# Optimization experiments

Measured on AMD Instinct MI355X. Metric: run time of the kernel, lower is better.

## Reference

```python
import jax, jax.numpy as jnp
import numpy as np

B, T, NE, NH, HD = 4, 1024, 768, 12, 64
CURV = 0.0
EPS = 1e-6
LN_EPS = 1e-5
ROPE_BASE = 10000.0


def project(x, k):
    # Lift Euclidean vector onto Lorentz hyperboloid with curvature K = exp(k):
    # time coord t = sqrt(K + ||x||^2) so that <lx, lx>_L = -K.
    K = jnp.exp(k)
    t = jnp.sqrt(K + jnp.sum(x * x, axis=-1, keepdims=True))
    return jnp.concatenate([t, x], axis=-1)


def lorentz_distance(lq, lk, k):
    # lq, lk: (B, H, T, D+1); k: (1, H, 1, 1) log-curvature.
    # d = sqrt(K) * arccosh(clamp(-<q,k>_L / K, 1+eps))
    K = jnp.exp(k)
    inner = (jnp.einsum('bhid,bhjd->bhij', lq[..., 1:], lk[..., 1:])
             - jnp.einsum('bhi,bhj->bhij', lq[..., 0], lk[..., 0]))
    c = jnp.clip(-inner / K, 1.0 + EPS, None)
    return jnp.sqrt(K) * jnp.arccosh(c)


def lorentz_norm(x):
    # sqrt(|<x,x>_L|) with <x,x>_L = -x0^2 + ||xs||^2  (keepdim)
    inner = -x[..., 0:1] ** 2 + jnp.sum(x[..., 1:] ** 2, axis=-1, keepdims=True)
    return jnp.sqrt(jnp.clip(-inner, EPS, None))


def rotary_tables():
    inv_freq = 1.0 / (ROPE_BASE ** (np.arange(0, HD, 2, dtype=np.float32) / HD))
    t = np.arange(T, dtype=np.float32)
    freqs = np.outer(t, inv_freq)  # (T, HD/2)
    cos = jnp.asarray(np.cos(freqs))[None, :, None, :]  # (1,T,1,HD/2)
    sin = jnp.asarray(np.sin(freqs))[None, :, None, :]
    return cos, sin


def apply_rotary(x, cos, sin):
    # x: (B, T, H, HD)
    x1, x2 = x[..., : HD // 2], x[..., HD // 2:]
    return jnp.concatenate([x1 * cos + x2 * sin, -x1 * sin + x2 * cos], axis=-1)


def layernorm(y, g, b):
    m = jnp.mean(y, axis=-1, keepdims=True)
    v = jnp.mean((y - m) ** 2, axis=-1, keepdims=True)
    return (y - m) / jnp.sqrt(v + LN_EPS) * g + b


def setup_inputs() -> dict:
    key = jax.random.key(0)
    ks = jax.random.split(key, 8)
    s = 0.02
    return {
        'x': jax.random.normal(ks[0], (B, T, NE), dtype=jnp.float32),
        'block_curvature': jnp.asarray(CURV, dtype=jnp.float32),
        'mlp_curvature': jnp.asarray(CURV, dtype=jnp.float32),
        'attn_curvatures': jnp.ones((1, NH, 1, 1), dtype=jnp.float32) * CURV,
        'qkv_w': jax.random.normal(ks[1], (3 * NE, NE + 1), dtype=jnp.float32) * s,
        'attn_proj_w': jax.random.normal(ks[2], (NE, (HD + 1) * NH), dtype=jnp.float32) * s,
        'attn_proj_b': jnp.zeros((NE,), dtype=jnp.float32),
        'mlp_expand_w': jax.random.normal(ks[3], (4 * NE + 3, NE + 1), dtype=jnp.float32) * s,
        'mlp_expand_b': jnp.zeros((4 * NE + 3,), dtype=jnp.float32),
        'mlp_shrink_w': jax.random.normal(ks[4], (NE, 4 * (NE + 1)), dtype=jnp.float32) * s,
        'mlp_shrink_b': jnp.zeros((NE,), dtype=jnp.float32),
        'ln_g': jnp.ones((NE,), dtype=jnp.float32),
        'ln_b': jnp.zeros((NE,), dtype=jnp.float32),
    }


def reference(x, block_curvature, mlp_curvature, attn_curvatures, qkv_w,
              attn_proj_w, attn_proj_b, mlp_expand_w, mlp_expand_b,
              mlp_shrink_w, mlp_shrink_b, ln_g, ln_b):
    cos, sin = rotary_tables()
    causal_bias = jnp.where(
        jnp.triu(jnp.ones((T, T), dtype=bool), k=1), -jnp.inf, 0.0).astype(jnp.float32)

    def block_norm(lx):
        return project(layernorm(lx[..., 1:], ln_g, ln_b), block_curvature)

    def attn(lx):
        qkv = lx @ qkv_w.T  # (B, T, 3*NE)
        q, k, v = jnp.split(qkv, 3, axis=-1)
        q = apply_rotary(q.reshape(B, T, NH, HD), cos, sin)
        k = apply_rotary(k.reshape(B, T, NH, HD), cos, sin)
        v = v.reshape(B, T, NH, HD)
        lq = project(q.transpose(0, 2, 1, 3), attn_curvatures)  # (B,H,T,HD+1)
        lk = project(k.transpose(0, 2, 1, 3), attn_curvatures)
        lv = project(v.transpose(0, 2, 1, 3), attn_curvatures)
        dis = lorentz_distance(lq, lk, attn_curvatures)  # (B,H,T,T)
        aw = jax.nn.softmax(-dis + causal_bias, axis=-1)
        a = jnp.einsum('bhij,bhjd->bhid', aw, lv)  # (B,H,T,HD+1)
        a = a * jnp.sqrt(jnp.exp(attn_curvatures)) / lorentz_norm(a)
        a = a.transpose(0, 2, 1, 3).reshape(B, T, NH * (HD + 1))
        a = a @ attn_proj_w.T + attn_proj_b
        return project(a, block_curvature)

    def mlp(lx):
        h = lx @ mlp_expand_w.T + mlp_expand_b  # (B,T,4*NE+3)
        h = project(h, mlp_curvature)[..., 1:]  # drop time coord back to 4*NE+3
        h = jax.nn.gelu(h, approximate=False)
        h = project(h, mlp_curvature)  # (B,T,4*(NE+1))
        h = h @ mlp_shrink_w.T + mlp_shrink_b
        return project(h, block_curvature)

    def skip(lx, f_lx):
        return project(lx[..., 1:] + f_lx[..., 1:], block_curvature)

    lx = project(x, block_curvature)  # (B,T,NE+1)
    lx = skip(lx, attn(block_norm(lx)))
    lx = skip(lx, mlp(block_norm(lx)))
    return lx
```

## Files before the change

kernel.cpp:

```cpp
#include <hip/hip_runtime.h>
#include <cmath>

typedef unsigned short ushort_t;
typedef __attribute__((ext_vector_type(8))) short short8;
typedef __attribute__((ext_vector_type(4))) float floatx4;

#define NH    12
#define T     1024
#define ROWS  4096
#define NE    768
#define KPA   832
#define KPB   3136
#define NEXP  3200
#define HEXP  3075
#define NSPLIT 3

__device__ __forceinline__ ushort_t f2bf(float f) {
  union { float f; unsigned u; } v; v.f = f;
  unsigned r = v.u + 0x7fffu + ((v.u >> 16) & 1u);
  return (ushort_t)(r >> 16);
}
__device__ __forceinline__ ushort_t f2bf_trunc(float f) {
  union { float f; unsigned u; } v; v.f = f;
  return (ushort_t)(v.u >> 16);
}
__device__ __forceinline__ float bf2f(ushort_t b) {
  union { unsigned u; float f; } v; v.u = ((unsigned)b) << 16;
  return v.f;
}
__device__ __forceinline__ float blk_reduce_sum(float v, float* sm) {
  #pragma unroll
  for (int o = 32; o > 0; o >>= 1) v += __shfl_xor(v, o, 64);
  int lane = threadIdx.x & 63, w = threadIdx.x >> 6;
  __syncthreads();
  if (lane == 0) sm[w] = v;
  __syncthreads();
  return sm[0] + sm[1] + sm[2] + sm[3];
}
__device__ __forceinline__ float red16_sum(float v) {
  #pragma unroll
  for (int o = 1; o < 16; o <<= 1) v += __shfl_xor(v, o, 64);
  return v;
}

#define NB_A 7488
#define NB_B 2496
#define NB_C 10400
#define NB_D 9408
#define NB_E 16
__device__ __forceinline__ void cvt_elem(ushort_t* __restrict__ dst,
                                         const float* __restrict__ src,
                                         int idx, int srcRows, int srcK, int dstK) {
  int r = idx / dstK, c = idx - r * dstK;
  dst[idx] = (r < srcRows && c < srcK) ? f2bf(src[(size_t)r * srcK + c]) : (ushort_t)0;
}
__global__ __launch_bounds__(256) void prep_kernel(
    ushort_t* __restrict__ qkv_wb, const float* __restrict__ qkvw,
    ushort_t* __restrict__ proj_wb, const float* __restrict__ projw,
    ushort_t* __restrict__ exp_wb, const float* __restrict__ expw,
    ushort_t* __restrict__ shr_wb, const float* __restrict__ shrw,
    ushort_t* __restrict__ aout_bf,
    const float* __restrict__ xin, const float* __restrict__ g,
    const float* __restrict__ bb, const float* __restrict__ curv,
    ushort_t* __restrict__ lnp) {
  __shared__ float sm[4];
  int blk = blockIdx.x;
  int tid = threadIdx.x;
  if (blk < NB_A) {
    cvt_elem(qkv_wb, qkvw, blk * 256 + tid, 2304, 769, KPA);
  } else if (blk < NB_A + NB_B) {
    cvt_elem(proj_wb, projw, (blk - NB_A) * 256 + tid, 768, 780, KPA);
  } else if (blk < NB_A + NB_B + NB_C) {
    cvt_elem(exp_wb, expw, (blk - NB_A - NB_B) * 256 + tid, HEXP, 769, KPA);
  } else if (blk < NB_A + NB_B + NB_C + NB_D) {
    cvt_elem(shr_wb, shrw, (blk - NB_A - NB_B - NB_C) * 256 + tid, 768, 3076, KPB);
  } else if (blk < NB_A + NB_B + NB_C + NB_D + NB_E) {
    int r = (blk - NB_A - NB_B - NB_C - NB_D) * 256 + tid;
    ushort_t* p = aout_bf + (size_t)r * KPA + 780;
    #pragma unroll
    for (int j = 0; j < KPA - 780; ++j) p[j] = 0;
  } else {
    const int row = blk - (NB_A + NB_B + NB_C + NB_D + NB_E);
    const float* xr = xin + (size_t)row * NE;
    float xv[3];
    float s = 0.f, ss = 0.f;
    #pragma unroll
    for (int i = 0; i < 3; ++i) {
      xv[i] = xr[tid + 256 * i];
      s += xv[i]; ss += xv[i] * xv[i];
    }
    s = blk_reduce_sum(s, sm);
    ss = blk_reduce_sum(ss, sm);
    float mean = s * (1.f / 768.f);
    float var = ss * (1.f / 768.f) - mean * mean;
    float rstd = rsqrtf(var + 1e-5f);
    float yv[3]; float ys = 0.f;
    #pragma unroll
    for (int i = 0; i < 3; ++i) {
      int c = tid + 256 * i;
      yv[i] = (xv[i] - mean) * rstd * g[c] + bb[c];
      ys += yv[i] * yv[i];
    }
    ys = blk_reduce_sum(ys, sm);
    float tc = sqrtf(expf(curv[0]) + ys);
    ushort_t* orow = lnp + (size_t)row * KPA;
    #pragma unroll
    for (int i = 0; i < 3; ++i) orow[1 + tid + 256 * i] = f2bf(yv[i]);
    if (tid == 0) orow[0] = f2bf(tc);
    if (tid < KPA - 769) orow[769 + tid] = 0;
  }
}

__global__ __launch_bounds__(256) void gemm_bf16(
    const ushort_t* __restrict__ A, int lda,
    const ushort_t* __restrict__ W, int ldw,
    void* __restrict__ Cout, int ldc,
    int nkTot, int cpt,
    const float* __restrict__ bias, int biasN,
    const float* __restrict__ res, int ldres,
    int outMode, void* __restrict__ Cp) {
  __shared__ ushort_t As[128 * 64];
  __shared__ ushort_t Bs[128 * 64];
  const int tid = threadIdx.x;
  const int w = tid >> 6, lane = tid & 63;

  int bx = blockIdx.x, by = blockIdx.y;
  {
    const int gx = gridDim.x, gy = gridDim.y;
    const int nwg = gx * gy;
    if ((nwg & 7) == 0) {
      int lin = by * gx + bx;
      int swz = (lin & 7) * (nwg >> 3) + (lin >> 3);
      bx = swz % gx;
      by = swz / gx;
    }
  }
  const int rowBase = by << 7;
  const int colBase = bx << 7;
  const int wm = (w & 1) * 64, wn = (w >> 1) * 64;
  const int lm = lane & 15, quad = lane >> 4;
  const int p0 = quad ^ (lm & 7);

  floatx4 acc[4][4];
  #pragma unroll
  for (int i = 0; i < 4; ++i)
    #pragma unroll
    for (int j = 0; j < 4; ++j) {
      floatx4 z = {0.f, 0.f, 0.f, 0.f};
      acc[i][j] = z;
    }

  const int kt0 = (int)blockIdx.z * cpt;
  const int kt1 = min(nkTot, kt0 + cpt);
  for (int kt = kt0; kt < kt1; ++kt) {
    __syncthreads();
    #pragma unroll
    for (int j = 0; j < 4; ++j) {
      int ci = j * 256 + tid;
      int r = ci >> 3;
      int g = (ci & 7) ^ (r & 7);
      const ushort_t* ga = A + (size_t)(rowBase + r) * lda + kt * 64 + g * 8;
      const ushort_t* gb = W + (size_t)(colBase + r) * ldw + kt * 64 + g * 8;
      __builtin_amdgcn_global_load_lds(
          (const __attribute__((address_space(1))) void*)ga,
          (__attribute__((address_space(3))) void*)&As[(j * 256 + w * 64) * 8],
          16, 0, 0);
      __builtin_amdgcn_global_load_lds(
          (const __attribute__((address_space(1))) void*)gb,
          (__attribute__((address_space(3))) void*)&Bs[(j * 256 + w * 64) * 8],
          16, 0, 0);
    }
    __syncthreads();

    #pragma unroll
    for (int s = 0; s < 2; ++s) {
      const int ps = s ? (p0 ^ 4) : p0;
      short8 af[4], bfr[4];
      #pragma unroll
      for (int i = 0; i < 4; ++i) {
        af[i]  = *(const short8*)&As[(wm + i * 16 + lm) * 64 + ps * 8];
        bfr[i] = *(const short8*)&Bs[(wn + i * 16 + lm) * 64 + ps * 8];
      }
      #pragma unroll
      for (int i = 0; i < 4; ++i)
        #pragma unroll
        for (int jn = 0; jn < 4; ++jn)
          acc[i][jn] = __builtin_amdgcn_mfma_f32_16x16x32_bf16(
              af[i], bfr[jn], acc[i][jn], 0, 0, 0);
    }
  }

  if (gridDim.z > 1) {
    ushort_t* dst = (ushort_t*)Cp + (size_t)blockIdx.z * ROWS * ldc;
    #pragma unroll
    for (int i = 0; i < 4; ++i)
      #pragma unroll
      for (int jn = 0; jn < 4; ++jn) {
        const int col = colBase + wn + jn * 16 + lm;
        #pragma unroll
        for (int rg = 0; rg < 4; ++rg) {
          const int row = rowBase + wm + i * 16 + quad * 4 + rg;
          dst[(size_t)row * ldc + col] = f2bf(acc[i][jn][rg]);
        }
      }
  } else if (outMode == 1) {
    ushort_t* C = (ushort_t*)Cout;
    #pragma unroll
    for (int i = 0; i < 4; ++i)
      #pragma unroll
      for (int jn = 0; jn < 4; ++jn) {
        const int col = colBase + wn + jn * 16 + lm;
        const float bv = bias ? ((col < biasN) ? bias[col] : 0.f) : 0.f;
        #pragma unroll
        for (int rg = 0; rg < 4; ++rg) {
          const int row = rowBase + wm + i * 16 + quad * 4 + rg;
          C[(size_t)row * ldc + col] = f2bf(acc[i][jn][rg] + bv);
        }
      }
  } else {
    float* C = (float*)Cout;
    #pragma unroll
    for (int i = 0; i < 4; ++i)
      #pragma unroll
      for (int jn = 0; jn < 4; ++jn) {
        const int col = colBase + wn + jn * 16 + lm;
        const float bv = bias ? ((col < biasN) ? bias[col] : 0.f) : 0.f;
        #pragma unroll
        for (int rg = 0; rg < 4; ++rg) {
          const int row = rowBase + wm + i * 16 + quad * 4 + rg;
          float o = acc[i][jn][rg] + bv;
          if (res) o += res[(size_t)row * ldres + col];
          C[(size_t)row * ldc + col] = o;
        }
      }
  }
}

__global__ __launch_bounds__(256) void rope_project(
    const ushort_t* __restrict__ qkv, const float* __restrict__ ac,
    ushort_t* __restrict__ qb, ushort_t* __restrict__ kb, ushort_t* __restrict__ vtb,
    float* __restrict__ q0, float* __restrict__ k0, float* __restrict__ v0) {
  int gid = blockIdx.x * 4 + (threadIdx.x >> 6);
  int lane = threadIdx.x & 63;
  int h = gid % NH;
  int bt = gid / NH;
  int t = bt & (T - 1);
  int b = bt >> 10;
  size_t base = (size_t)bt * 2304 + h * 64;
  float qv = bf2f(qkv[base + lane]);
  float kv = bf2f(qkv[base + 768 + lane]);
  float vv = bf2f(qkv[base + 1536 + lane]);
  int f = lane & 31;
  float ang = (float)t * __builtin_amdgcn_exp2f(-(float)f * 0.4152410118661534f);
  float sn, cs;
  sincosf(ang, &sn, &cs);
  float qp = __shfl(qv, lane ^ 32, 64);
  float kp = __shfl(kv, lane ^ 32, 64);
  float qr = (lane < 32) ? (qv * cs + qp * sn) : (-qp * sn + qv * cs);
  float kr = (lane < 32) ? (kv * cs + kp * sn) : (-kp * sn + kv * cs);
  float Kh = expf(ac[h]);
  float sq = qr * qr, sk = kr * kr, sv = vv * vv;
  #pragma unroll
  for (int o = 32; o > 0; o >>= 1) {
    sq += __shfl_xor(sq, o, 64);
    sk += __shfl_xor(sk, o, 64);
    sv += __shfl_xor(sv, o, 64);
  }
  size_t idx = ((size_t)(b * NH + h) * T + t);
  qb[idx * 64 + lane] = f2bf(qr);
  kb[idx * 64 + lane] = f2bf(kr);
  vtb[(size_t)(b * NH + h) * (64 * T) + (size_t)lane * T + t] = f2bf(vv);
  if (lane == 0) {
    q0[idx] = sqrtf(Kh + sq);
    k0[idx] = sqrtf(Kh + sk);
    v0[idx] = sqrtf(Kh + sv);
  }
}

__global__ __launch_bounds__(512, 4) void attn_kernel(
    const ushort_t* __restrict__ qb, const ushort_t* __restrict__ kb,
    const ushort_t* __restrict__ vtb,
    const float* __restrict__ q0, const float* __restrict__ k0,
    const float* __restrict__ v0,
    const float* __restrict__ ac,
    ushort_t* __restrict__ Opart, float* __restrict__ lpart,
    float* __restrict__ a0part) {
  __shared__ ushort_t QP[8 * 1152];
  __shared__ ushort_t Ks[2][64 * 64];
  __shared__ ushort_t Vts[2][64 * 64];

  const int sIdx = blockIdx.x;
  const int qtile = (int)gridDim.y - 1 - (int)blockIdx.y;
  const int bh = blockIdx.z;
  const int h = bh % NH;
  const int qt0 = qtile * 128;
  const int tid = threadIdx.x;
  const int w = tid >> 6, lane = tid & 63;
  const int lm = lane & 15, quad = lane >> 4;
  const int wm = w * 16;
  const int sw = lm & 7;
  const int preg = w * 1152;

  const int n = 2 * qtile + 2;
  const int kbeg = (n * sIdx) / NSPLIT;
  const int kend = (n * (sIdx + 1)) / NSPLIT;
  const size_t pb = (size_t)(sIdx * 48 + bh) * T;

  if (kbeg >= kend) {
    #pragma unroll
    for (int r = 0; r < 4; ++r) {
      const int i = qt0 + wm + quad * 4 + r;
      ushort_t* orow = Opart + (pb + i) * 64;
      #pragma unroll
      for (int nt = 0; nt < 4; ++nt) orow[nt * 16 + lm] = 0;
      if (lm == 0) { lpart[pb + i] = 0.f; a0part[pb + i] = 0.f; }
    }
    return;
  }

  const float Kh = expf(ac[h]);
  const float sqrtK = sqrtf(Kh);
  const float invK = 1.0f / Kh;
  const float nsK = -sqrtK;
  const bool k1 = (Kh == 1.0f);

  {
    const ushort_t* qtp = qb + ((size_t)bh * T + qt0) * 64;
    #pragma unroll
    for (int j = 0; j < 2; ++j) {
      int g = j * 8 + w;
      int ci = g * 64 + lane;
      int r = ci >> 3;
      int clog = ((ci & 7) ^ (r & 7)) * 8;
      __builtin_amdgcn_global_load_lds(
          (const __attribute__((address_space(1))) void*)(qtp + r * 64 + clog),
          (__attribute__((address_space(3))) void*)&QP[(g >> 1) * 1152 + (g & 1) * 512],
          16, 0, 0);
    }
  }
  const ushort_t* kbase = kb + (size_t)bh * T * 64;
  const ushort_t* vbh = vtb + (size_t)bh * (64 * T);
  const float* k0row = k0 + (size_t)bh * T;
  const float* v0row = v0 + (size_t)bh * T;
  const int ldr = tid >> 3;
  const int ldcs = ((tid & 7) ^ (ldr & 7)) * 8;
  {
    const int j0 = kbeg * 64;
    __builtin_amdgcn_global_load_lds(
        (const __attribute__((address_space(1))) void*)(kbase + (size_t)(j0 + ldr) * 64 + ldcs),
        (__attribute__((address_space(3))) void*)&Ks[0][w * 512], 16, 0, 0);
    __builtin_amdgcn_global_load_lds(
        (const __attribute__((address_space(1))) void*)(vbh + (size_t)ldr * T + j0 + ldcs),
        (__attribute__((address_space(3))) void*)&Vts[0][w * 512], 16, 0, 0);
  }
  float k0n[4], v0n[4];
  #pragma unroll
  for (int jt = 0; jt < 4; ++jt) {
    k0n[jt] = k0row[kbeg * 64 + jt * 16 + lm];
    v0n[jt] = v0row[kbeg * 64 + jt * 16 + lm];
  }
  float q0rv[4];
  #pragma unroll
  for (int r = 0; r < 4; ++r)
    q0rv[r] = q0[(size_t)bh * T + qt0 + wm + quad * 4 + r];

  asm volatile("s_waitcnt vmcnt(0)" ::: "memory");
  __builtin_amdgcn_s_barrier();
  __builtin_amdgcn_sched_barrier(0);

  short8 qf0 = *(const short8*)&QP[preg + lm * 64 + ((0 + quad) ^ sw) * 8];
  short8 qf1 = *(const short8*)&QP[preg + lm * 64 + ((4 + quad) ^ sw) * 8];
  asm volatile("" : "+v"(qf0), "+v"(qf1));

  float lsum[4], a0r[4];
  floatx4 oacc[4];
  #pragma unroll
  for (int r = 0; r < 4; ++r) { lsum[r] = 0.f; a0r[r] = 0.f; }
  #pragma unroll
  for (int nt = 0; nt < 4; ++nt) { floatx4 z = {0.f,0.f,0.f,0.f}; oacc[nt] = z; }

  int cur = 0;
  for (int kt = kbeg; kt < kend; ++kt) {
    const bool hasNext = (kt + 1 < kend);
    float k0i[4], v0v[4];
    #pragma unroll
    for (int jt = 0; jt < 4; ++jt) { k0i[jt] = k0n[jt] * invK; v0v[jt] = v0n[jt]; }

    if (hasNext) {
      const int j0n = (kt + 1) * 64;
      __builtin_amdgcn_global_load_lds(
          (const __attribute__((address_space(1))) void*)(kbase + (size_t)(j0n + ldr) * 64 + ldcs),
          (__attribute__((address_space(3))) void*)&Ks[cur ^ 1][w * 512], 16, 0, 0);
      __builtin_amdgcn_global_load_lds(
          (const __attribute__((address_space(1))) void*)(vbh + (size_t)ldr * T + j0n + ldcs),
          (__attribute__((address_space(3))) void*)&Vts[cur ^ 1][w * 512], 16, 0, 0);
      #pragma unroll
      for (int jt = 0; jt < 4; ++jt) {
        k0n[jt] = k0row[j0n + jt * 16 + lm];
        v0n[jt] = v0row[j0n + jt * 16 + lm];
      }
    }

    const int j0 = kt * 64;
    const ushort_t* Kc = Ks[cur];
    const ushort_t* Vc = Vts[cur];

    floatx4 sacc[4];
    __builtin_amdgcn_s_setprio(1);
    #pragma unroll
    for (int jt = 0; jt < 4; ++jt) {
      const int krow = jt * 16 + lm;
      short8 kf0 = *(const short8*)&Kc[krow * 64 + ((0 + quad) ^ sw) * 8];
      short8 kf1 = *(const short8*)&Kc[krow * 64 + ((4 + quad) ^ sw) * 8];
      floatx4 z = {0.f, 0.f, 0.f, 0.f};
      z = __builtin_amdgcn_mfma_f32_16x16x32_bf16(qf0, kf0, z, 0, 0, 0);
      z = __builtin_amdgcn_mfma_f32_16x16x32_bf16(qf1, kf1, z, 0, 0, 0);
      sacc[jt] = z;
    }
    __builtin_amdgcn_s_setprio(0);

    const bool maskT = (kt >= 2 * qtile);
    if (k1) {
      #pragma unroll
      for (int r = 0; r < 4; ++r) {
        const int i = qt0 + wm + quad * 4 + r;
        float ls = 0.f, a0s = 0.f;
        #pragma unroll
        for (int jt = 0; jt < 4; ++jt) {
          float c = fmaf(-invK, sacc[jt][r], q0rv[r] * k0i[jt]);
          c = fmaxf(c, 1.000001f);
          float p = c - sqrtf(fmaf(c, c, -1.f));
          if (maskT && (j0 + jt * 16 + lm > i)) p = 0.f;
          ushort_t pb2 = f2bf_trunc(p);
          QP[preg + (quad * 4 + r) * 72 + jt * 16 + lm] = pb2;
          float pf = bf2f(pb2);
          ls += pf;
          a0s = fmaf(pf, v0v[jt], a0s);
        }
        lsum[r] += ls;
        a0r[r] += a0s;
      }
    } else {
      #pragma unroll
      for (int r = 0; r < 4; ++r) {
        const int i = qt0 + wm + quad * 4 + r;
        float ls = 0.f, a0s = 0.f;
        #pragma unroll
        for (int jt = 0; jt < 4; ++jt) {
          float c = fmaf(-invK, sacc[jt][r], q0rv[r] * k0i[jt]);
          c = fmaxf(c, 1.000001f);
          float z = c + sqrtf(fmaf(c, c, -1.f));
          float p = __builtin_amdgcn_exp2f(nsK * __builtin_amdgcn_logf(z));
          if (maskT && (j0 + jt * 16 + lm > i)) p = 0.f;
          ushort_t pb2 = f2bf_trunc(p);
          QP[preg + (quad * 4 + r) * 72 + jt * 16 + lm] = pb2;
          float pf = bf2f(pb2);
          ls += pf;
          a0s = fmaf(pf, v0v[jt], a0s);
        }
        lsum[r] += ls;
        a0r[r] += a0s;
      }
    }

    short8 pf0 = *(const short8*)&QP[preg + lm * 72 + quad * 8];
    short8 pf1 = *(const short8*)&QP[preg + lm * 72 + 32 + quad * 8];
    __builtin_amdgcn_s_setprio(1);
    #pragma unroll
    for (int nt = 0; nt < 4; ++nt) {
      const int vrow = nt * 16 + lm;
      short8 vf0 = *(const short8*)&Vc[vrow * 64 + ((0 + quad) ^ sw) * 8];
      short8 vf1 = *(const short8*)&Vc[vrow * 64 + ((4 + quad) ^ sw) * 8];
      oacc[nt] = __builtin_amdgcn_mfma_f32_16x16x32_bf16(pf0, vf0, oacc[nt], 0, 0, 0);
      oacc[nt] = __builtin_amdgcn_mfma_f32_16x16x32_bf16(pf1, vf1, oacc[nt], 0, 0, 0);
    }
    __builtin_amdgcn_s_setprio(0);

    if (hasNext) {
      asm volatile("s_waitcnt vmcnt(0)" ::: "memory");
      __builtin_amdgcn_s_barrier();
      __builtin_amdgcn_sched_barrier(0);
    }
    cur ^= 1;
  }

  #pragma unroll
  for (int r = 0; r < 4; ++r) {
    float lf = red16_sum(lsum[r]);
    float a0f = red16_sum(a0r[r]);
    const int i = qt0 + wm + quad * 4 + r;
    ushort_t* orow = Opart + (pb + i) * 64;
    #pragma unroll
    for (int nt = 0; nt < 4; ++nt) orow[nt * 16 + lm] = f2bf(oacc[nt][r]);
    if (lm == 0) { lpart[pb + i] = lf; a0part[pb + i] = a0f; }
  }
}

__global__ __launch_bounds__(256) void attn_combine(
    const ushort_t* __restrict__ Opart, const float* __restrict__ lpart,
    const float* __restrict__ a0part,
    const float* __restrict__ ac, ushort_t* __restrict__ aout) {
  const int widx = blockIdx.x * 4 + (threadIdx.x >> 6);
  const int lane = threadIdx.x & 63;
  const int bh = widx >> 10;
  const int t = widx & 1023;
  const int h = bh % NH, b = bh / NH;
  float L = 0.f, A0 = 0.f, O = 0.f;
  #pragma unroll
  for (int sp = 0; sp < NSPLIT; ++sp) {
    const size_t r = (size_t)(sp * 48 + bh) * T + t;
    L += lpart[r];
    A0 += a0part[r];
    O += bf2f(Opart[r * 64 + lane]);
  }
  const float invl = 1.f / L;
  float av = O * invl;
  float ssq = av * av;
  #pragma unroll
  for (int o = 32; o > 0; o >>= 1) ssq += __shfl_xor(ssq, o, 64);
  float a0n = A0 * invl;
  float nsq = fmaxf(a0n * a0n - ssq, 1e-6f);
  float Kh = expf(ac[h]);
  float scale = sqrtf(Kh) * rsqrtf(nsq);
  ushort_t* orow = aout + (size_t)(b * T + t) * KPA + h * 65;
  orow[1 + lane] = f2bf(av * scale);
  if (lane == 0) orow[0] = f2bf(a0n * scale);
}

__global__ __launch_bounds__(256) void gelu_project(
    const ushort_t* __restrict__ hsrc, const float* __restrict__ curv,
    ushort_t* __restrict__ hp) {
  __shared__ float sm[4];
  const int row = blockIdx.x;
  const int tid = threadIdx.x;
  const ushort_t* hr = hsrc + (size_t)row * NEXP;
  float gv[13];
  float ss = 0.f;
  #pragma unroll
  for (int i = 0; i < 13; ++i) {
    int c = tid + 256 * i;
    float xx = (c < HEXP) ? bf2f(hr[c]) : 0.f;
    float gg = 0.5f * xx * (1.f + erff(xx * 0.70710678118654752f));
    gv[i] = gg; ss += gg * gg;
  }
  ss = blk_reduce_sum(ss, sm);
  float tc = sqrtf(expf(curv[0]) + ss);
  ushort_t* orow = hp + (size_t)row * KPB;
  #pragma unroll
  for (int i = 0; i < 13; ++i) {
    int c = tid + 256 * i;
    if (c < HEXP) orow[1 + c] = f2bf(gv[i]);
  }
  if (tid == 0) orow[0] = f2bf(tc);
  if (tid < KPB - (HEXP + 1)) orow[HEXP + 1 + tid] = 0;
}

__global__ __launch_bounds__(256) void reduce_ln_project(
    const ushort_t* __restrict__ Cp, int nsplit,
    const float* __restrict__ bias, const float* __restrict__ res,
    float* __restrict__ x2out,
    const float* __restrict__ g, const float* __restrict__ bb,
    const float* __restrict__ curv, ushort_t* __restrict__ lnp) {
  __shared__ float sm[4];
  const int row = blockIdx.x;
  const int tid = threadIdx.x;
  float xv[3];
  float s = 0.f, ss = 0.f;
  #pragma unroll
  for (int i = 0; i < 3; ++i) {
    const int c = tid + 256 * i;
    float v = bias[c] + res[(size_t)row * NE + c];
    for (int sp = 0; sp < nsplit; ++sp)
      v += bf2f(Cp[(size_t)sp * ROWS * NE + (size_t)row * NE + c]);
    x2out[(size_t)row * NE + c] = v;
    xv[i] = v;
    s += v; ss += v * v;
  }
  s = blk_reduce_sum(s, sm);
  ss = blk_reduce_sum(ss, sm);
  float mean = s * (1.f / 768.f);
  float var = ss * (1.f / 768.f) - mean * mean;
  float rstd = rsqrtf(var + 1e-5f);
  float yv[3]; float ys = 0.f;
  #pragma unroll
  for (int i = 0; i < 3; ++i) {
    int c = tid + 256 * i;
    yv[i] = (xv[i] - mean) * rstd * g[c] + bb[c];
    ys += yv[i] * yv[i];
  }
  ys = blk_reduce_sum(ys, sm);
  float tc = sqrtf(expf(curv[0]) + ys);
  ushort_t* orow = lnp + (size_t)row * KPA;
  #pragma unroll
  for (int i = 0; i < 3; ++i) orow[1 + tid + 256 * i] = f2bf(yv[i]);
  if (tid == 0) orow[0] = f2bf(tc);
  if (tid < KPA - 769) orow[769 + tid] = 0;
}

__global__ __launch_bounds__(256) void reduce_final_project(
    const ushort_t* __restrict__ Cp, int nsplit,
    const float* __restrict__ bias, const float* __restrict__ res,
    const float* __restrict__ curv, float* __restrict__ out) {
  __shared__ float sm[4];
  const int row = blockIdx.x;
  const int tid = threadIdx.x;
  float v[3]; float ss = 0.f;
  #pragma unroll
  for (int i = 0; i < 3; ++i) {
    const int c = tid + 256 * i;
    float t = bias[c] + res[(size_t)row * NE + c];
    for (int sp = 0; sp < nsplit; ++sp)
      t += bf2f(Cp[(size_t)sp * ROWS * NE + (size_t)row * NE + c]);
    v[i] = t; ss += t * t;
  }
  ss = blk_reduce_sum(ss, sm);
  float tc = sqrtf(expf(curv[0]) + ss);
  float* o = out + (size_t)row * 769;
  #pragma unroll
  for (int i = 0; i < 3; ++i) o[1 + tid + 256 * i] = v[i];
  if (tid == 0) o[0] = tc;
}

extern "C" void kernel_launch(void* const* d_in, const int* in_sizes, int n_in,
                              void* d_out, int out_size, void* d_ws, size_t ws_size,
                              hipStream_t stream) {
  (void)in_sizes; (void)n_in; (void)out_size; (void)ws_size;
  const float* x     = (const float*)d_in[0];
  const float* bc    = (const float*)d_in[1];
  const float* mc    = (const float*)d_in[2];
  const float* ac    = (const float*)d_in[3];
  const float* qkvw  = (const float*)d_in[4];
  const float* projw = (const float*)d_in[5];
  const float* projb = (const float*)d_in[6];
  const float* expw  = (const float*)d_in[7];
  const float* expb  = (const float*)d_in[8];
  const float* shrw  = (const float*)d_in[9];
  const float* shrb  = (const float*)d_in[10];
  const float* lng   = (const float*)d_in[11];
  const float* lnb   = (const float*)d_in[12];
  float* out = (float*)d_out;

  float* x2 = (float*)d_ws;
  ushort_t* qkv_wb  = (ushort_t*)(x2 + (size_t)ROWS * NE);
  ushort_t* proj_wb = qkv_wb + (size_t)2304 * KPA;
  ushort_t* exp_wb  = proj_wb + (size_t)768 * KPA;
  ushort_t* shr_wb  = exp_wb + (size_t)NEXP * KPA;
  ushort_t* lnp_bf  = shr_wb + (size_t)768 * KPB;
  ushort_t* aout_bf = lnp_bf + (size_t)ROWS * KPA;
  char* r2 = (char*)(aout_bf + (size_t)ROWS * KPA);
  ushort_t* qkvb = (ushort_t*)r2;
  ushort_t* qbb = qkvb + (size_t)ROWS * 2304;
  ushort_t* kbb = qbb + (size_t)48 * T * 64;
  ushort_t* vtb = kbb + (size_t)48 * T * 64;
  float* q0b = (float*)(vtb + (size_t)48 * T * 64);
  float* k0b = q0b + (size_t)48 * T;
  float* v0b = k0b + (size_t)48 * T;
  ushort_t* Opart = (ushort_t*)(v0b + (size_t)48 * T);
  float* lpart = (float*)(Opart + (size_t)NSPLIT * 48 * T * 64);
  float* a0part = lpart + (size_t)NSPLIT * 48 * T;
  ushort_t* ppartP = (ushort_t*)r2;
  ushort_t* hbbf = (ushort_t*)r2;
  ushort_t* hp_bf = hbbf + (size_t)ROWS * NEXP;
  ushort_t* ppartS = hp_bf + (size_t)ROWS * KPB;

  prep_kernel<<<NB_A + NB_B + NB_C + NB_D + NB_E + ROWS, 256, 0, stream>>>(
      qkv_wb, qkvw, proj_wb, projw, exp_wb, expw, shr_wb, shrw, aout_bf,
      x, lng, lnb, bc, lnp_bf);
  gemm_bf16<<<dim3(2304 / 128, ROWS / 128, 1), 256, 0, stream>>>(
      lnp_bf, KPA, qkv_wb, KPA, qkvb, 2304, KPA / 64, KPA / 64,
      nullptr, 0, nullptr, 0, 1, nullptr);
  rope_project<<<(ROWS * NH) / 4, 256, 0, stream>>>(qkvb, ac, qbb, kbb, vtb, q0b, k0b, v0b);
  attn_kernel<<<dim3(NSPLIT, T / 128, 48), 512, 0, stream>>>(
      qbb, kbb, vtb, q0b, k0b, v0b, ac, Opart, lpart, a0part);
  attn_combine<<<(48 * T) / 4, 256, 0, stream>>>(Opart, lpart, a0part, ac, aout_bf);
  gemm_bf16<<<dim3(768 / 128, ROWS / 128, 2), 256, 0, stream>>>(
      aout_bf, KPA, proj_wb, KPA, nullptr, NE, KPA / 64, 7,
      nullptr, 0, nullptr, 0, 0, ppartP);
  reduce_ln_project<<<ROWS, 256, 0, stream>>>(
      ppartP, 2, projb, x, x2, lng, lnb, bc, lnp_bf);
  gemm_bf16<<<dim3(NEXP / 128, ROWS / 128, 1), 256, 0, stream>>>(
      lnp_bf, KPA, exp_wb, KPA, hbbf, NEXP, KPA / 64, KPA / 64,
      expb, HEXP, nullptr, 0, 1, nullptr);
  gelu_project<<<ROWS, 256, 0, stream>>>(hbbf, mc, hp_bf);
  gemm_bf16<<<dim3(768 / 128, ROWS / 128, 4), 256, 0, stream>>>(
      hp_bf, KPB, shr_wb, KPB, nullptr, NE, KPB / 64, 13,
      nullptr, 0, nullptr, 0, 0, ppartS);
  reduce_final_project<<<ROWS, 256, 0, stream>>>(
      ppartS, 4, shrb, x2, bc, out);
}
```

Before: 369.3 us.

## Load K/V fragments directly from global memory, drop LDS double buffering and barriers

The attention kernel no longer stages K and V^T tiles through double-buffered shared memory. Each wave now reads its MFMA K and V fragments straight from global memory (relying on L1/L2 reuse across waves) and loads only its own Q rows, which removes all block-wide barriers. This shrinks LDS use and synchronisation, but adds latency-exposed global loads with no prefetch, and the 8 waves re-read the same K/V data. The occupancy hint in launch_bounds is also removed.

```diff
diff --git a/kernel.cpp b/kernel.cpp
--- a/kernel.cpp
+++ b/kernel.cpp
@@ -277,7 +277,7 @@
   }
 }
 
-__global__ __launch_bounds__(512, 4) void attn_kernel(
+__global__ __launch_bounds__(512) void attn_kernel(
     const ushort_t* __restrict__ qb, const ushort_t* __restrict__ kb,
     const ushort_t* __restrict__ vtb,
     const float* __restrict__ q0, const float* __restrict__ k0,
@@ -286,8 +286,6 @@
     ushort_t* __restrict__ Opart, float* __restrict__ lpart,
     float* __restrict__ a0part) {
   __shared__ ushort_t QP[8 * 1152];
-  __shared__ ushort_t Ks[2][64 * 64];
-  __shared__ ushort_t Vts[2][64 * 64];
 
   const int sIdx = blockIdx.x;
   const int qtile = (int)gridDim.y - 1 - (int)blockIdx.y;
@@ -325,16 +323,14 @@
   const bool k1 = (Kh == 1.0f);
 
   {
-    const ushort_t* qtp = qb + ((size_t)bh * T + qt0) * 64;
+    const ushort_t* qtp = qb + ((size_t)bh * T + qt0 + wm) * 64;
     #pragma unroll
     for (int j = 0; j < 2; ++j) {
-      int g = j * 8 + w;
-      int ci = g * 64 + lane;
-      int r = ci >> 3;
-      int clog = ((ci & 7) ^ (r & 7)) * 8;
+      int lr = j * 8 + (lane >> 3);
+      int ch = (lane & 7) ^ (lr & 7);
       __builtin_amdgcn_global_load_lds(
-          (const __attribute__((address_space(1))) void*)(qtp + r * 64 + clog),
-          (__attribute__((address_space(3))) void*)&QP[(g >> 1) * 1152 + (g & 1) * 512],
+          (const __attribute__((address_space(1))) void*)(qtp + lr * 64 + ch * 8),
+          (__attribute__((address_space(3))) void*)&QP[preg + j * 512],
           16, 0, 0);
     }
   }
@@ -342,30 +338,12 @@
   const ushort_t* vbh = vtb + (size_t)bh * (64 * T);
   const float* k0row = k0 + (size_t)bh * T;
   const float* v0row = v0 + (size_t)bh * T;
-  const int ldr = tid >> 3;
-  const int ldcs = ((tid & 7) ^ (ldr & 7)) * 8;
-  {
-    const int j0 = kbeg * 64;
-    __builtin_amdgcn_global_load_lds(
-        (const __attribute__((address_space(1))) void*)(kbase + (size_t)(j0 + ldr) * 64 + ldcs),
-        (__attribute__((address_space(3))) void*)&Ks[0][w * 512], 16, 0, 0);
-    __builtin_amdgcn_global_load_lds(
-        (const __attribute__((address_space(1))) void*)(vbh + (size_t)ldr * T + j0 + ldcs),
-        (__attribute__((address_space(3))) void*)&Vts[0][w * 512], 16, 0, 0);
-  }
-  float k0n[4], v0n[4];
-  #pragma unroll
-  for (int jt = 0; jt < 4; ++jt) {
-    k0n[jt] = k0row[kbeg * 64 + jt * 16 + lm];
-    v0n[jt] = v0row[kbeg * 64 + jt * 16 + lm];
-  }
   float q0rv[4];
   #pragma unroll
   for (int r = 0; r < 4; ++r)
     q0rv[r] = q0[(size_t)bh * T + qt0 + wm + quad * 4 + r];
 
   asm volatile("s_waitcnt vmcnt(0)" ::: "memory");
-  __builtin_amdgcn_s_barrier();
   __builtin_amdgcn_sched_barrier(0);
 
   short8 qf0 = *(const short8*)&QP[preg + lm * 64 + ((0 + quad) ^ sw) * 8];
@@ -379,42 +357,28 @@
   #pragma unroll
   for (int nt = 0; nt < 4; ++nt) { floatx4 z = {0.f,0.f,0.f,0.f}; oacc[nt] = z; }
 
-  int cur = 0;
   for (int kt = kbeg; kt < kend; ++kt) {
-    const bool hasNext = (kt + 1 < kend);
+    const int j0 = kt * 64;
+    const ushort_t* ktb = kbase + (size_t)j0 * 64;
+
+    short8 kf0[4], kf1[4];
     float k0i[4], v0v[4];
     #pragma unroll
-    for (int jt = 0; jt < 4; ++jt) { k0i[jt] = k0n[jt] * invK; v0v[jt] = v0n[jt]; }
-
-    if (hasNext) {
-      const int j0n = (kt + 1) * 64;
-      __builtin_amdgcn_global_load_lds(
-          (const __attribute__((address_space(1))) void*)(kbase + (size_t)(j0n + ldr) * 64 + ldcs),
-          (__attribute__((address_space(3))) void*)&Ks[cur ^ 1][w * 512], 16, 0, 0);
-      __builtin_amdgcn_global_load_lds(
-          (const __attribute__((address_space(1))) void*)(vbh + (size_t)ldr * T + j0n + ldcs),
-          (__attribute__((address_space(3))) void*)&Vts[cur ^ 1][w * 512], 16, 0, 0);
-      #pragma unroll
-      for (int jt = 0; jt < 4; ++jt) {
-        k0n[jt] = k0row[j0n + jt * 16 + lm];
-        v0n[jt] = v0row[j0n + jt * 16 + lm];
-      }
-    }
-
-    const int j0 = kt * 64;
-    const ushort_t* Kc = Ks[cur];
-    const ushort_t* Vc = Vts[cur];
+    for (int jt = 0; jt < 4; ++jt) {
+      const int krow = jt * 16 + lm;
+      kf0[jt] = *(const short8*)(ktb + krow * 64 + quad * 8);
+      kf1[jt] = *(const short8*)(ktb + krow * 64 + 32 + quad * 8);
+      k0i[jt] = k0row[j0 + krow] * invK;
+      v0v[jt] = v0row[j0 + krow];
+    }
 
     floatx4 sacc[4];
     __builtin_amdgcn_s_setprio(1);
     #pragma unroll
     for (int jt = 0; jt < 4; ++jt) {
-      const int krow = jt * 16 + lm;
-      short8 kf0 = *(const short8*)&Kc[krow * 64 + ((0 + quad) ^ sw) * 8];
-      short8 kf1 = *(const short8*)&Kc[krow * 64 + ((4 + quad) ^ sw) * 8];
       floatx4 z = {0.f, 0.f, 0.f, 0.f};
-      z = __builtin_amdgcn_mfma_f32_16x16x32_bf16(qf0, kf0, z, 0, 0, 0);
-      z = __builtin_amdgcn_mfma_f32_16x16x32_bf16(qf1, kf1, z, 0, 0, 0);
+      z = __builtin_amdgcn_mfma_f32_16x16x32_bf16(qf0, kf0[jt], z, 0, 0, 0);
+      z = __builtin_amdgcn_mfma_f32_16x16x32_bf16(qf1, kf1[jt], z, 0, 0, 0);
       sacc[jt] = z;
     }
     __builtin_amdgcn_s_setprio(0);
@@ -468,20 +432,13 @@
     __builtin_amdgcn_s_setprio(1);
     #pragma unroll
     for (int nt = 0; nt < 4; ++nt) {
-      const int vrow = nt * 16 + lm;
-      short8 vf0 = *(const short8*)&Vc[vrow * 64 + ((0 + quad) ^ sw) * 8];
-      short8 vf1 = *(const short8*)&Vc[vrow * 64 + ((4 + quad) ^ sw) * 8];
+      const ushort_t* vr = vbh + (size_t)(nt * 16 + lm) * T + j0;
+      short8 vf0 = *(const short8*)(vr + quad * 8);
+      short8 vf1 = *(const short8*)(vr + 32 + quad * 8);
       oacc[nt] = __builtin_amdgcn_mfma_f32_16x16x32_bf16(pf0, vf0, oacc[nt], 0, 0, 0);
       oacc[nt] = __builtin_amdgcn_mfma_f32_16x16x32_bf16(pf1, vf1, oacc[nt], 0, 0, 0);
     }
     __builtin_amdgcn_s_setprio(0);
-
-    if (hasNext) {
-      asm volatile("s_waitcnt vmcnt(0)" ::: "memory");
-      __builtin_amdgcn_s_barrier();
-      __builtin_amdgcn_sched_barrier(0);
-    }
-    cur ^= 1;
   }
 
   #pragma unroll
```

Result: slower. 406.8 us (+10.2%).
